# Optimization experiments

Measured on AMD Instinct MI355X. Metric: run time of the kernel, lower is better.

The kernel has to match this reference:

```python
import jax, jax.numpy as jnp
import numpy as np

# LSS config: nuScenes-standard grid/frustum
B, N, D, C = 8, 6, 41, 64          # batch, cameras, depth bins, cam feature channels
OGH, OGW = 256, 704                # final image dims
FH, FW = OGH // 16, OGW // 16      # feature map dims after downsample=16 -> 16, 44
DX = np.array([0.5, 0.5, 20.0], np.float32)      # voxel sizes from gen_dx_bx
BX = np.array([-49.75, -49.75, 0.0], np.float32) # voxel grid offsets (lower + dx/2)
NX = (200, 200, 1)                                # voxel counts (x, y, z)


def _make_cam_rots():
    # camera-to-ego: cam z-forward -> ego x-forward, plus per-camera yaw
    base = np.array([[0., 0., 1.], [-1., 0., 0.], [0., -1., 0.]], np.float32)
    rots = []
    for n in range(N):
        yaw = 2.0 * np.pi * n / N
        Rz = np.array([[np.cos(yaw), -np.sin(yaw), 0.], [np.sin(yaw), np.cos(yaw), 0.], [0., 0., 1.]], np.float32)
        rots.append(Rz @ base)
    return np.stack(rots)


def setup_inputs() -> dict:
    key = jax.random.key(0)
    k1, k2, k3 = jax.random.split(key, 3)
    feat = jax.random.normal(k1, (B, N, D + C, FH, FW), jnp.float32)  # depthnet output
    rots = jnp.broadcast_to(jnp.asarray(_make_cam_rots())[None], (B, N, 3, 3))
    trans = jax.random.uniform(k2, (B, N, 3), jnp.float32, -1.5, 1.5)
    f = 550.0
    intr = np.array([[f, 0., OGW / 2.], [0., f, OGH / 2.], [0., 0., 1.]], np.float32)
    intrins = jnp.broadcast_to(jnp.asarray(intr)[None, None], (B, N, 3, 3))
    post_rots = jnp.broadcast_to(jnp.eye(3, dtype=jnp.float32)[None, None], (B, N, 3, 3))
    post_trans = jax.random.uniform(k3, (B, N, 3), jnp.float32, -2.0, 2.0)
    return dict(feat=feat, rots=rots, trans=trans, intrins=intrins,
                post_rots=post_rots, post_trans=post_trans)


def _frustum():
    ds = jnp.arange(4.0, 45.0, 1.0)               # (D,)
    xs = jnp.linspace(0.0, OGW - 1.0, FW)
    ys = jnp.linspace(0.0, OGH - 1.0, FH)
    ds_ = jnp.broadcast_to(ds[:, None, None], (D, FH, FW))
    xs_ = jnp.broadcast_to(xs[None, None, :], (D, FH, FW))
    ys_ = jnp.broadcast_to(ys[None, :, None], (D, FH, FW))
    return jnp.stack([xs_, ys_, ds_], -1)          # (D, FH, FW, 3)


def reference(feat, rots, trans, intrins, post_rots, post_trans):
    # --- get_geometry: frustum points -> ego frame, (B,N,D,FH,FW,3) ---
    frustum = _frustum()
    pts = frustum[None, None] - post_trans[:, :, None, None, None, :]
    pts = jnp.einsum('bnij,bndhwj->bndhwi', jnp.linalg.inv(post_rots), pts)
    pts = jnp.concatenate([pts[..., :2] * pts[..., 2:3], pts[..., 2:3]], -1)  # unproject
    combine = rots @ jnp.linalg.inv(intrins)
    geom = jnp.einsum('bnij,bndhwj->bndhwi', combine, pts) + trans[:, :, None, None, None, :]

    # --- get_depth_feat: softmax depth dist outer-product with cam features ---
    depth = jax.nn.softmax(feat[:, :, :D], axis=2)           # (B,N,D,FH,FW)
    x = depth[:, :, None] * feat[:, :, D:, None]             # (B,N,C,D,FH,FW)
    x = jnp.transpose(x, (0, 1, 3, 4, 5, 2))                 # (B,N,D,FH,FW,C)

    # --- voxel_pooling: scatter-add points into BEV grid (== sort + cumsum trick) ---
    dx = jnp.asarray(DX); bx = jnp.asarray(BX)
    g = ((geom - (bx - dx / 2.0)) / dx).astype(jnp.int32)    # (B,N,D,FH,FW,3) voxel ix
    kept = ((g[..., 0] >= 0) & (g[..., 0] < NX[0]) &
            (g[..., 1] >= 0) & (g[..., 1] < NX[1]) &
            (g[..., 2] >= 0) & (g[..., 2] < NX[2]))
    gx = jnp.clip(g[..., 0], 0, NX[0] - 1)
    gy = jnp.clip(g[..., 1], 0, NX[1] - 1)
    gz = jnp.clip(g[..., 2], 0, NX[2] - 1)
    bidx = jnp.broadcast_to(jnp.arange(B, dtype=jnp.int32)[:, None, None, None, None], kept.shape)
    nseg = B * NX[2] * NX[0] * NX[1]
    vox = ((bidx * NX[2] + gz) * NX[0] + gx) * NX[1] + gy
    seg = jnp.where(kept, vox, nseg).reshape(-1)             # dropped pts -> dummy bin
    xf = x.reshape(-1, C)                                    # (Nprime, C)
    pooled = jax.ops.segment_sum(xf, seg, num_segments=nseg + 1)[:nseg]
    bev = pooled.reshape(B, NX[2], NX[0], NX[1], C)
    # torch: final (B,C,Z,X,Y) then cat(unbind(dim=2), 1) -> (B, Z*C, X, Y), z-major
    bev = jnp.transpose(bev, (0, 1, 4, 2, 3)).reshape(B, NX[2] * C, NX[0], NX[1])
    return bev
```

## Files before the change

### kernel.cpp

```cpp
#include <hip/hip_runtime.h>
#include <math.h>

#define B_   8
#define N_   6
#define D_   41
#define C_   64
#define FH_  16
#define FW_  44
#define HW_  (FH_*FW_)
#define CHW_ ((D_+C_)*FH_*FW_)
#define NPIX (B_*N_*FH_*FW_)
#define NPT  (NPIX*D_)
#define NXV  200
#define NYV  200
#define NCOL (B_*N_*FW_)
#define FEATBLKS (B_*N_*FH_)
#define SPW  24
#define SPC  48
#define NREC (NCOL*SPC)
#define NBUCK (B_*NXV*2)
#define CAP  512

__device__ __forceinline__ float mul_(float a, float b){ return __fmul_rn(a,b); }
__device__ __forceinline__ float add_(float a, float b){ return __fadd_rn(a,b); }
__device__ __forceinline__ float sub_(float a, float b){ return __fsub_rn(a,b); }

__device__ void inv3(const float* A, float* X){
  float U[3][3];
  float L[3][3] = {{1.f,0.f,0.f},{0.f,1.f,0.f},{0.f,0.f,1.f}};
  int p[3] = {0,1,2};
  #pragma unroll
  for (int i=0;i<3;i++)
    #pragma unroll
    for (int j=0;j<3;j++) U[i][j] = A[i*3+j];
  #pragma unroll
  for (int k=0;k<3;k++){
    int pr = k; float mx = fabsf(U[k][k]);
    #pragma unroll
    for (int r=0;r<3;r++){
      if (r > k){ float v = fabsf(U[r][k]); if (v > mx){ mx = v; pr = r; } }
    }
    if (pr != k){
      #pragma unroll
      for (int j=0;j<3;j++){ float t=U[k][j]; U[k][j]=U[pr][j]; U[pr][j]=t; }
      #pragma unroll
      for (int j=0;j<3;j++){ if (j<k){ float t=L[k][j]; L[k][j]=L[pr][j]; L[pr][j]=t; } }
      int t=p[k]; p[k]=p[pr]; p[pr]=t;
    }
    #pragma unroll
    for (int r=0;r<3;r++){
      if (r > k){
        float m = __fdiv_rn(U[r][k], U[k][k]);
        L[r][k] = m;
        #pragma unroll
        for (int j=0;j<3;j++){ if (j>k) U[r][j] = sub_(U[r][j], mul_(m, U[k][j])); }
      }
    }
  }
  #pragma unroll
  for (int col=0; col<3; col++){
    float y[3];
    #pragma unroll
    for (int i=0;i<3;i++) y[i] = (p[i]==col) ? 1.f : 0.f;
    #pragma unroll
    for (int i=1;i<3;i++)
      #pragma unroll
      for (int j=0;j<3;j++){ if (j<i) y[i] = sub_(y[i], mul_(L[i][j], y[j])); }
    float x[3];
    #pragma unroll
    for (int i=2;i>=0;i--){
      float t = y[i];
      #pragma unroll
      for (int j=0;j<3;j++){ if (j>i) t = sub_(t, mul_(U[i][j], x[j])); }
      x[i] = __fdiv_rn(t, U[i][i]);
    }
    X[0*3+col]=x[0]; X[1*3+col]=x[1]; X[2*3+col]=x[2];
  }
}

__device__ void cam_params(const float* __restrict__ rots, const float* __restrict__ trans,
                           const float* __restrict__ intrins, const float* __restrict__ post_rots,
                           const float* __restrict__ post_trans, int t, float* o){
  float invK[9], invP[9];
  inv3(intrins + t*9, invK);
  inv3(post_rots + t*9, invP);
  const float* R = rots + t*9;
  #pragma unroll
  for (int i=0;i<9;i++) o[i] = invP[i];
  #pragma unroll
  for (int i=0;i<3;i++)
    #pragma unroll
    for (int j=0;j<3;j++){
      float s = mul_(R[i*3+0], invK[0*3+j]);
      s = add_(s, mul_(R[i*3+1], invK[1*3+j]));
      s = add_(s, mul_(R[i*3+2], invK[2*3+j]));
      o[9 + i*3+j] = s;
    }
  o[18]=post_trans[t*3+0]; o[19]=post_trans[t*3+1]; o[20]=post_trans[t*3+2];
  o[21]=trans[t*3+0];      o[22]=trans[t*3+1];      o[23]=trans[t*3+2];
}

__device__ __forceinline__ int point_vox(const float* __restrict__ cp,
                                         int h, int w, int d){
  float u = mul_((float)w, 703.0f/43.0f);
  float v = mul_((float)h, 17.0f);
  float p0 = sub_(u, cp[18]);
  float p1 = sub_(v, cp[19]);
  float a0 = add_(mul_(cp[0],p0), mul_(cp[1],p1));
  float a1 = add_(mul_(cp[3],p0), mul_(cp[4],p1));
  float a2 = add_(mul_(cp[6],p0), mul_(cp[7],p1));
  float dd = add_(4.0f, (float)d);
  float p2 = sub_(dd, cp[20]);
  float r0 = add_(a0, mul_(cp[2],p2));
  float r1 = add_(a1, mul_(cp[5],p2));
  float r2 = add_(a2, mul_(cp[8],p2));
  float q0 = mul_(r0, r2), q1 = mul_(r1, r2), q2 = r2;
  float g0 = add_(add_(add_(mul_(cp[9], q0), mul_(cp[10],q1)), mul_(cp[11],q2)), cp[21]);
  float g1 = add_(add_(add_(mul_(cp[12],q0), mul_(cp[13],q1)), mul_(cp[14],q2)), cp[22]);
  float g2 = add_(add_(add_(mul_(cp[15],q0), mul_(cp[16],q1)), mul_(cp[17],q2)), cp[23]);
  float bxq = mul_(sub_(g0, -50.0f), 2.0f);
  float byq = mul_(sub_(g1, -50.0f), 2.0f);
  float bzq = __fdiv_rn(sub_(g2, -10.0f), 20.0f);
  int gx=(int)bxq, gy=(int)byq, gz=(int)bzq;
  if ((gx>=0)&(gx<NXV)&(gy>=0)&(gy<NYV)&(gz==0))
    return (gx<<8) | gy;
  return -1;
}

__global__ __launch_bounds__(256) void lss_featprep(const float* __restrict__ feat,
    const float* __restrict__ rots, const float* __restrict__ trans,
    const float* __restrict__ intrins, const float* __restrict__ post_rots,
    const float* __restrict__ post_trans,
    float* __restrict__ featT, float* __restrict__ dprobA,
    unsigned short* __restrict__ segA, int* __restrict__ bcnt){
  int bid = blockIdx.x;
  int tid = threadIdx.x;
  if (bid >= FEATBLKS){
    for (int i = tid; i < NBUCK; i += 256) bcnt[i] = 0;
    return;
  }
  __shared__ float lds[D_+C_][FW_+1];
  __shared__ float ssum[FW_];
  __shared__ float cam[24];
  int h = bid & 15, bn = bid >> 4;
  if (tid == 0)
    cam_params(rots, trans, intrins, post_rots, post_trans, bn, cam);
  const float* fb = feat + (size_t)bn*CHW_ + h*FW_;
  for (int i = tid; i < (D_+C_)*FW_; i += 256){
    int ch = i / FW_, w = i - ch*FW_;
    lds[ch][w] = fb[(size_t)ch*HW_ + w];
  }
  __syncthreads();
  if (tid < FW_){
    float m = lds[0][tid];
    for (int d = 1; d < D_; d++) m = fmaxf(m, lds[d][tid]);
    float s = 0.f;
    for (int d = 0; d < D_; d++){ float e = expf(lds[d][tid] - m); lds[d][tid] = e; s += e; }
    ssum[tid] = s;
  }
  __syncthreads();
  int pix0 = bid * FW_;
  for (int i = tid; i < C_*FW_; i += 256){
    int w = i >> 6, c = i & 63;
    featT[(size_t)(pix0 + w)*C_ + c] = lds[D_ + c][w];
  }
  for (int i = tid; i < D_*FW_; i += 256){
    int w = i / D_, d = i - w*D_;
    int pix = pix0 + w;
    dprobA[(size_t)pix*D_ + d] = __fdiv_rn(lds[d][w], ssum[w]);
    int v = point_vox(cam, h, w, d);
    segA[(size_t)pix*D_ + d] = (v < 0) ? 0xFFFFu : (unsigned short)v;
  }
}

__global__ __launch_bounds__(256) void lss_cols(const float* __restrict__ featT,
    const unsigned short* __restrict__ segA, const float* __restrict__ dprobA,
    float* __restrict__ payload, int* __restrict__ bcnt, unsigned* __restrict__ bidx){
  __shared__ __align__(16) float dpmT[2][D_][16];
  __shared__ unsigned vmin[2][D_];
  int col0 = blockIdx.x*2;
  int tid = threadIdx.x, lane = tid & 63, wv = tid >> 6;
  for (int i = tid; i < 2*D_; i += 256) ((unsigned*)vmin)[i] = 0xFFFFFFFFu;
  __syncthreads();
  for (int i = tid; i < 2*16*D_; i += 256){
    int c = i / (16*D_);
    int r = i - c*(16*D_);
    int h = r / D_, d = r - h*D_;
    int col = col0 + c;
    int w = col % FW_, bn = col / FW_;
    size_t g = (size_t)((bn*HW_ + w) + h*FW_)*D_ + d;
    unsigned s = segA[g];
    float dp = dprobA[g];
    dpmT[c][d][h] = (s == 0xFFFFu) ? 0.f : dp;
    if (s != 0xFFFFu) atomicMin(&vmin[c][d], s);
  }
  __syncthreads();
  int cw = wv >> 1, dw = wv & 1;
  int col = col0 + cw;
  int w = col % FW_, bn = col / FW_;
  int b = bn / N_;
  int pixbase = bn*HW_ + w;
  float fT[16];
  #pragma unroll
  for (int h = 0; h < 16; h++)
    fT[h] = featT[(size_t)(pixbase + h*FW_)*C_ + lane];
  int d0 = dw ? 21 : 0;
  int d1 = dw ? D_ : 21;
  int slotbase = col*SPC + dw*SPW;
  int cnt = 0;
  unsigned curv = 0xFFFFFFFFu; float acc = 0.f;
  for (int d = d0; d < d1; d++){
    unsigned vd = vmin[cw][d];
    if (vd > 60000u) continue;
    if (vd != curv){
      if (curv != 0xFFFFFFFFu && cnt < SPW){
        int slot = slotbase + cnt;
        payload[(size_t)slot*C_ + lane] = acc;
        if (lane == 0){
          int bucket = (b*NXV + (int)(curv >> 8))*2 + ((int)(curv & 0xFFu) >= 100);
          int pos = atomicAdd(&bcnt[bucket], 1);
          if (pos < CAP)
            bidx[(size_t)bucket*CAP + pos] = ((unsigned)slot << 8) | (curv & 0xFFu);
        }
        cnt++;
      }
      curv = vd; acc = 0.f;
    }
    const float4* q = (const float4*)dpmT[cw][d];
    float4 q0 = q[0], q1 = q[1], q2 = q[2], q3 = q[3];
    acc = fmaf(q0.x, fT[0],  acc); acc = fmaf(q0.y, fT[1],  acc);
    acc = fmaf(q0.z, fT[2],  acc); acc = fmaf(q0.w, fT[3],  acc);
    acc = fmaf(q1.x, fT[4],  acc); acc = fmaf(q1.y, fT[5],  acc);
    acc = fmaf(q1.z, fT[6],  acc); acc = fmaf(q1.w, fT[7],  acc);
    acc = fmaf(q2.x, fT[8],  acc); acc = fmaf(q2.y, fT[9],  acc);
    acc = fmaf(q2.z, fT[10], acc); acc = fmaf(q2.w, fT[11], acc);
    acc = fmaf(q3.x, fT[12], acc); acc = fmaf(q3.y, fT[13], acc);
    acc = fmaf(q3.z, fT[14], acc); acc = fmaf(q3.w, fT[15], acc);
  }
  if (curv != 0xFFFFFFFFu && cnt < SPW){
    int slot = slotbase + cnt;
    payload[(size_t)slot*C_ + lane] = acc;
    if (lane == 0){
      int bucket = (b*NXV + (int)(curv >> 8))*2 + ((int)(curv & 0xFFu) >= 100);
      int pos = atomicAdd(&bcnt[bucket], 1);
      if (pos < CAP)
        bidx[(size_t)bucket*CAP + pos] = ((unsigned)slot << 8) | (curv & 0xFFu);
    }
  }
}

__global__ __launch_bounds__(256) void lss_out(const float* __restrict__ payload,
    const int* __restrict__ bcnt, const unsigned* __restrict__ bidx,
    float* __restrict__ out){
  __shared__ float tile[100][C_+1];
  __shared__ unsigned qb[CAP];
  int bid = blockIdx.x;
  int half = bid & 1;
  int x = (bid >> 1) % NXV;
  int b = bid / (NXV*2);
  int tid = threadIdx.x, lane = tid & 63, wv = tid >> 6;
  const float4 z4 = make_float4(0.f,0.f,0.f,0.f);
  for (int i = tid; i < 100*(C_+1)/4; i += 256) ((float4*)tile)[i] = z4;
  int n = bcnt[bid]; if (n > CAP) n = CAP;
  for (int i = tid; i < n; i += 256) qb[i] = bidx[(size_t)bid*CAP + i];
  __syncthreads();
  for (int r = 0; r < n; r++){
    unsigned e = qb[r];
    int yl = (int)(e & 0xFFu) - half*100;
    if ((unsigned)yl < 100u && (yl & 3) == wv){
      int slot = (int)(e >> 8);
      if (slot < NREC){
        float v = payload[(size_t)slot*C_ + lane];
        tile[yl][lane] += v;
      }
    }
  }
  __syncthreads();
  size_t obase = ((size_t)(b*C_)*NXV + x)*NYV + half*100;
  for (int i = tid; i < C_*100; i += 256){
    int c = i / 100, y = i - c*100;
    out[obase + (size_t)c*(NXV*NYV) + y] = tile[y][c];
  }
}

__global__ void lss_prep(const float* __restrict__ rots, const float* __restrict__ trans,
                         const float* __restrict__ intrins, const float* __restrict__ post_rots,
                         const float* __restrict__ post_trans, float* __restrict__ cam){
  int t = threadIdx.x;
  if (t >= B_*N_) return;
  cam_params(rots, trans, intrins, post_rots, post_trans, t, cam + t*24);
}

__global__ __launch_bounds__(256) void lss_scatter_fb(const float* __restrict__ feat,
    const float* __restrict__ cam, float* __restrict__ pooled){
  int wave = threadIdx.x >> 6, lane = threadIdx.x & 63;
  int pix = blockIdx.x*4 + wave;
  if (pix >= NPIX) return;
  int w = pix % FW_; int t = pix / FW_;
  int h = t % FH_;   int bn = t / FH_;
  int b = bn / N_;
  const float* fb = feat + (size_t)bn*CHW_ + h*FW_ + w;
  float logit = (lane < D_) ? fb[(size_t)lane*HW_] : -INFINITY;
  float mx = logit;
  #pragma unroll
  for (int o=32;o;o>>=1) mx = fmaxf(mx, __shfl_xor(mx,o));
  float e = (lane < D_) ? expf(logit - mx) : 0.f;
  float ssum = e;
  #pragma unroll
  for (int o=32;o;o>>=1) ssum += __shfl_xor(ssum,o);
  float dprob = e / ssum;
  float fc = fb[(size_t)(D_+lane)*HW_];
  for (int d=0; d<D_; d++){
    int v = point_vox(cam + bn*24, h, w, d);
    if (v >= 0){
      int gx = v >> 8, gy = v & 0xFF;
      float dp = __shfl(dprob, d);
      atomicAdd(&pooled[(((size_t)(b*C_ + lane))*NXV + gx)*NYV + gy], mul_(dp, fc));
    }
  }
}

extern "C" void kernel_launch(void* const* d_in, const int* in_sizes, int n_in,
                              void* d_out, int out_size, void* d_ws, size_t ws_size,
                              hipStream_t stream) {
  const float* feat       = (const float*)d_in[0];
  const float* rots       = (const float*)d_in[1];
  const float* trans      = (const float*)d_in[2];
  const float* intrins    = (const float*)d_in[3];
  const float* post_rots  = (const float*)d_in[4];
  const float* post_trans = (const float*)d_in[5];
  float* out = (float*)d_out;

  char* p = (char*)d_ws;
  float*          featT   = (float*)p;          p += (size_t)NPIX*C_*4;
  float*          dprobA  = (float*)p;          p += (size_t)NPT*4;
  unsigned short* segA    = (unsigned short*)p; p += (size_t)NPT*2;
  float*          payload = (float*)p;          p += (size_t)NREC*C_*4;
  int*            bcnt    = (int*)p;            p += (size_t)NBUCK*4;
  unsigned*       bidx    = (unsigned*)p;       p += (size_t)NBUCK*CAP*4;
  size_t need = (size_t)(p - (char*)d_ws);

  if (ws_size < need){
    (void)hipMemsetAsync(d_out, 0, (size_t)out_size*sizeof(float), stream);
    lss_prep<<<1, 64, 0, stream>>>(rots, trans, intrins, post_rots, post_trans, (float*)d_ws);
    lss_scatter_fb<<<NPIX/4, 256, 0, stream>>>(feat, (float*)d_ws, out);
    return;
  }

  lss_featprep<<<FEATBLKS + 1, 256, 0, stream>>>(
      feat, rots, trans, intrins, post_rots, post_trans, featT, dprobA, segA, bcnt);
  lss_cols<<<NCOL/2, 256, 0, stream>>>(featT, segA, dprobA, payload, bcnt, bidx);
  lss_out<<<NBUCK, 256, 0, stream>>>(payload, bcnt, bidx, out);
}
```

Baseline: 82.17 us.

## Restructure BEV output pooling into 4-row by 16-channel tiles with LDS atomics

Changes the final gather kernel so each block covers four x-rows and a 16-channel group, rather than one half-row across all 64 channels. Bucket entries are spread across 16 sub-groups of threads that accumulate into shared memory with atomics. This replaces the serial per-entry loop, where one wave of four did useful work per record. Writes to the output become contiguous 800-float runs per channel. The trade-off is that each payload record is read by four separate blocks, one per channel group, at 64-byte granularity, and shared-memory atomics are added.

```diff
diff --git a/kernel.cpp b/kernel.cpp
--- a/kernel.cpp
+++ b/kernel.cpp
@@ -252,34 +252,39 @@
 __global__ __launch_bounds__(256) void lss_out(const float* __restrict__ payload,
     const int* __restrict__ bcnt, const unsigned* __restrict__ bidx,
     float* __restrict__ out){
-  __shared__ float tile[100][C_+1];
-  __shared__ unsigned qb[CAP];
+  __shared__ float tile[4][NYV][17];
   int bid = blockIdx.x;
-  int half = bid & 1;
-  int x = (bid >> 1) % NXV;
-  int b = bid / (NXV*2);
-  int tid = threadIdx.x, lane = tid & 63, wv = tid >> 6;
+  int cg = bid & 3;
+  int x4 = (bid >> 2) % 50;
+  int b  = bid / 200;
+  int x0 = x4*4;
+  int tid = threadIdx.x;
+  int sub = tid >> 4;
+  int cl  = tid & 15;
   const float4 z4 = make_float4(0.f,0.f,0.f,0.f);
-  for (int i = tid; i < 100*(C_+1)/4; i += 256) ((float4*)tile)[i] = z4;
-  int n = bcnt[bid]; if (n > CAP) n = CAP;
-  for (int i = tid; i < n; i += 256) qb[i] = bidx[(size_t)bid*CAP + i];
-  __syncthreads();
-  for (int r = 0; r < n; r++){
-    unsigned e = qb[r];
-    int yl = (int)(e & 0xFFu) - half*100;
-    if ((unsigned)yl < 100u && (yl & 3) == wv){
+  for (int i = tid; i < 4*NYV*17/4; i += 256) ((float4*)tile)[i] = z4;
+  __syncthreads();
+  #pragma unroll
+  for (int kb = 0; kb < 8; kb++){
+    int xl = kb >> 1;
+    int bk = (b*NXV + x0 + xl)*2 + (kb & 1);
+    int n = bcnt[bk]; if (n > CAP) n = CAP;
+    for (int r = sub; r < n; r += 16){
+      unsigned e = bidx[(size_t)bk*CAP + r];
       int slot = (int)(e >> 8);
-      if (slot < NREC){
-        float v = payload[(size_t)slot*C_ + lane];
-        tile[yl][lane] += v;
-      }
-    }
-  }
-  __syncthreads();
-  size_t obase = ((size_t)(b*C_)*NXV + x)*NYV + half*100;
-  for (int i = tid; i < C_*100; i += 256){
-    int c = i / 100, y = i - c*100;
-    out[obase + (size_t)c*(NXV*NYV) + y] = tile[y][c];
+      int gy   = (int)(e & 0xFFu);
+      if (slot < NREC && gy < NYV)
+        atomicAdd(&tile[xl][gy][cl],
+                  payload[(size_t)slot*C_ + cg*16 + cl]);
+    }
+  }
+  __syncthreads();
+  size_t obase = (((size_t)(b*C_ + cg*16))*NXV + x0)*NYV;
+  for (int i = tid; i < 16*4*NYV; i += 256){
+    int cc = i / 800;
+    int r  = i - cc*800;
+    int xl = r / NYV, y = r - xl*NYV;
+    out[obase + (size_t)cc*(NXV*NYV) + r] = tile[xl][y][cc];
   }
 }
 
@@ -350,5 +355,5 @@
   lss_featprep<<<FEATBLKS + 1, 256, 0, stream>>>(
       feat, rots, trans, intrins, post_rots, post_trans, featT, dprobA, segA, bcnt);
   lss_cols<<<NCOL/2, 256, 0, stream>>>(featT, segA, dprobA, payload, bcnt, bidx);
-  lss_out<<<NBUCK, 256, 0, stream>>>(payload, bcnt, bidx, out);
-}
+  lss_out<<<B_*50*4, 256, 0, stream>>>(payload, bcnt, bidx, out);
+}
```

Measured after the change: 109.0 us. 1.33x slower.
